# Optimization experiments

Hardware: AMD Instinct MI355X
Metric: run time of the kernel (lower is better)

Reference implementation:

```python
import jax, jax.numpy as jnp
import numpy as np

E = 2048      # embed_dim
H = 16        # num_heads
HD = E // H // 2   # differential head dim = 64
S = 2048      # seq len
B = 1         # batch
DEPTH = 12
LAMBDA_INIT = 0.8 - 0.6 * float(np.exp(-0.3 * DEPTH))
EPS = 1e-5


def setup_inputs() -> dict:
    key = jax.random.key(0)
    ks = jax.random.split(key, 12)
    n = lambda k, shape, s=1.0: (jax.random.normal(k, shape, dtype=jnp.float32) * s)
    return {
        "query": n(ks[0], (S, B, E)),
        "key": n(ks[1], (S, B, E)),
        "value": n(ks[2], (S, B, E)),
        "rel_pos": 0,
        "attn_mask": jnp.zeros((B, S), dtype=jnp.bool_),
        "Wq": n(ks[3], (E, E), 0.02),
        "Wk": n(ks[4], (E, E), 0.02),
        "Wv": n(ks[5], (E, E), 0.02),
        "Wo": n(ks[6], (E, E), 0.02),
        "lq1": n(ks[7], (HD,), 0.1),
        "lk1": n(ks[8], (HD,), 0.1),
        "lq2": n(ks[9], (HD,), 0.1),
        "lk2": n(ks[10], (HD,), 0.1),
        "subln_g": jnp.ones((2 * HD,), dtype=jnp.float32),
    }


def reference(query, key, value, rel_pos, attn_mask,
              Wq, Wk, Wv, Wo, lq1, lk1, lq2, lk2, subln_g):
    # (S,B,E) -> (B,S,E)
    q = jnp.einsum("sbe,fe->bsf", query, Wq)
    k = jnp.einsum("sbe,fe->bsf", key, Wk)
    v = jnp.einsum("sbe,fe->bsf", value, Wv)

    bsz, tgt_len, _ = q.shape
    scaling = HD ** -0.5

    q = q.reshape(bsz, tgt_len, 2 * H, HD).transpose(0, 2, 1, 3) * scaling  # (B,2H,S,hd)
    k = k.reshape(bsz, tgt_len, 2 * H, HD).transpose(0, 2, 1, 3)            # (B,2H,S,hd)
    v = v.reshape(bsz, tgt_len, H, 2 * HD).transpose(0, 2, 1, 3)            # (B,H,S,2hd)

    scores = jnp.einsum("bhqd,bhkd->bhqk", q, k)  # (B,2H,S,S)
    mask = jnp.where(attn_mask[:, None, None, :], -jnp.inf, 0.0).astype(scores.dtype)
    scores = jnp.nan_to_num(scores + mask)  # torch.nan_to_num: nan->0, -inf->finite min

    probs = jax.nn.softmax(scores.astype(jnp.float32), axis=-1).astype(scores.dtype)
    probs = jnp.clip(probs, -1e6, 1e6)  # clamp as in original (dropout is identity in eval)

    lam1 = jnp.exp(jnp.sum(lq1 * lk1))
    lam2 = jnp.exp(jnp.sum(lq2 * lk2))
    lam_full = lam1 - lam2 + LAMBDA_INIT

    probs = probs.reshape(bsz, H, 2, tgt_len, tgt_len)
    diff = probs[:, :, 0] - lam_full * probs[:, :, 1]   # (B,H,S,S)

    attn = jnp.einsum("bhqk,bhkd->bhqd", diff, v)       # (B,H,S,2hd)

    # RMSNorm over last dim with affine weight
    rms = jax.lax.rsqrt(jnp.mean(jnp.square(attn), axis=-1, keepdims=True) + EPS)
    attn = attn * rms * subln_g
    attn = attn * (1.0 - LAMBDA_INIT)

    attn = attn.transpose(0, 2, 1, 3).reshape(bsz, tgt_len, H * 2 * HD)  # (B,S,E)
    attn = attn.transpose(1, 0, 2)                                       # (S,B,E)
    return jnp.einsum("sbe,fe->sbf", attn, Wo)
```

## Files before the change

kernel.cpp:

```cpp
#include <hip/hip_runtime.h>
#include <stdint.h>

#define LAMBDA_INIT_F 0.7836057665f

typedef __bf16 bf16x8 __attribute__((ext_vector_type(8)));
typedef float  f32x4  __attribute__((ext_vector_type(4)));
typedef unsigned short u16x8 __attribute__((ext_vector_type(8)));
typedef unsigned short u16x4 __attribute__((ext_vector_type(4)));
typedef unsigned int u32x4 __attribute__((ext_vector_type(4)));

__device__ __forceinline__ unsigned short f2b(float f) {
    union { float f; unsigned u; } v; v.f = f;
    unsigned u = v.u;
    return (unsigned short)((u + 0x7fffu + ((u >> 16) & 1u)) >> 16);
}

__device__ __forceinline__ unsigned pk2(float a, float b) {
    unsigned ua = __float_as_uint(a) + 0x8000u;
    unsigned ub = __float_as_uint(b) + 0x8000u;
    return __builtin_amdgcn_perm(ub, ua, 0x07060302u);
}

#if __has_builtin(__builtin_amdgcn_exp2f)
#define EXP2(x) __builtin_amdgcn_exp2f(x)
#else
__device__ __forceinline__ float EXP2(float x) {
    float r; asm volatile("v_exp_f32 %0, %1\n\ts_nop 1" : "=v"(r) : "v"(x)); return r;
}
#endif

#define GLD16(gp, sp) __builtin_amdgcn_global_load_lds( \
    (const __attribute__((address_space(1))) void*)(uintptr_t)(gp), \
    (__attribute__((address_space(3))) void*)(uint32_t)(uintptr_t)(sp), 16, 0, 0)

__global__ __launch_bounds__(256) void cvt7(const float* __restrict__ s0, const float* __restrict__ s1,
                                            const float* __restrict__ s2, const float* __restrict__ s3,
                                            const float* __restrict__ s4, const float* __restrict__ s5,
                                            const float* __restrict__ s6,
                                            unsigned short* __restrict__ dst) {
    int z = blockIdx.y;
    const float* s = z == 0 ? s0 : z == 1 ? s1 : z == 2 ? s2 : z == 3 ? s3 : z == 4 ? s4 : z == 5 ? s5 : s6;
    unsigned short* d = dst + (size_t)z * 4194304;
    size_t i = ((size_t)blockIdx.x * 256 + threadIdx.x) * 8;
    float4 a = *(const float4*)(s + i);
    float4 b = *(const float4*)(s + i + 4);
    u16x8 o;
    o[0] = f2b(a.x); o[1] = f2b(a.y); o[2] = f2b(a.z); o[3] = f2b(a.w);
    o[4] = f2b(b.x); o[5] = f2b(b.y); o[6] = f2b(b.z); o[7] = f2b(b.w);
    *(u16x8*)(d + i) = o;
}

__global__ __launch_bounds__(512, 2) void gemm_qkv(const unsigned short* __restrict__ Abase,
                                                   const unsigned short* __restrict__ Bbase,
                                                   unsigned short* __restrict__ Cb,
                                                   unsigned short* __restrict__ VT,
                                                   float alpha0) {
    __shared__ __align__(16) unsigned short As[16384];
    __shared__ __align__(16) unsigned short Bs[16384];
    const int tid = threadIdx.x;
    const int wid = tid >> 6, lane = tid & 63;
    const int quad = lane >> 4, l16 = lane & 15;
    const int wr = wid >> 2, wc = wid & 3;
    const int bid = blockIdx.x;
    const int wrk = (bid & 7) * 24 + (bid >> 3);
    const int z = wrk >> 6;
    const int t6 = wrk & 63;
    const int m0 = (t6 >> 3) * 256, n0 = (t6 & 7) * 256;
    const unsigned short* A = Abase + (size_t)z * 4194304;
    const unsigned short* B = Bbase + (size_t)z * 4194304;
    const float alpha = (z == 0) ? alpha0 : 1.0f;

    const int sr = lane >> 2;
    const int sc = (((lane & 3) ^ ((lane >> 3) & 3)) * 8);
    const int rsw = ((l16 >> 1) & 3);

    f32x4 acc[8][4];
#pragma unroll
    for (int mi = 0; mi < 8; ++mi)
#pragma unroll
        for (int ni = 0; ni < 4; ++ni) acc[mi][ni] = f32x4{0.f, 0.f, 0.f, 0.f};

    auto STAGE_AH = [&](int h, int k0) {
        const int rowbase = (wid >> 2) * 128 + (wid & 3) * 16 + h * 64;
#pragma unroll
        for (int kk = 0; kk < 2; ++kk)
            GLD16(A + (size_t)(m0 + rowbase + sr) * 2048 + k0 + kk * 32 + sc, &As[(kk * 256 + rowbase) * 32]);
    };
    auto STAGE_BH = [&](int h, int k0) {
        const int rowbase = (wid >> 1) * 64 + (wid & 1) * 16 + h * 32;
#pragma unroll
        for (int kk = 0; kk < 2; ++kk)
            GLD16(B + (size_t)(n0 + rowbase + sr) * 2048 + k0 + kk * 32 + sc, &Bs[(kk * 256 + rowbase) * 32]);
    };

#define LD_A(mh, i, kk) (*(const bf16x8*)&As[(kk * 256 + wr * 128 + (mh) * 64 + (i) * 16 + l16) * 32 + (quad ^ rsw) * 8])
#define LD_B(nh, jn, kk) (*(const bf16x8*)&Bs[(kk * 256 + wc * 64 + (nh) * 32 + (jn) * 16 + l16) * 32 + (quad ^ rsw) * 8])

    STAGE_AH(0, 0); STAGE_BH(0, 0);
    STAGE_BH(1, 0);
    STAGE_AH(1, 0);
    asm volatile("s_waitcnt vmcnt(4)" ::: "memory");
    __builtin_amdgcn_s_barrier();

    for (int kt = 0; kt < 32; ++kt) {
        const int k1 = (kt + 1) * 64;
        bf16x8 af[2][4], b0[2][2], b1[2][2];

#pragma unroll
        for (int kk = 0; kk < 2; ++kk) {
#pragma unroll
            for (int i = 0; i < 4; ++i) af[kk][i] = LD_A(0, i, kk);
#pragma unroll
            for (int jn = 0; jn < 2; ++jn) b0[kk][jn] = LD_B(0, jn, kk);
        }
        __builtin_amdgcn_s_barrier();
        __builtin_amdgcn_s_setprio(1);
#pragma unroll
        for (int i = 0; i < 4; ++i)
#pragma unroll
            for (int jn = 0; jn < 2; ++jn)
#pragma unroll
                for (int kk = 0; kk < 2; ++kk)
                    acc[i][jn] = __builtin_amdgcn_mfma_f32_16x16x32_bf16(af[kk][i], b0[kk][jn], acc[i][jn], 0, 0, 0);
        __builtin_amdgcn_s_setprio(0);
        asm volatile("s_waitcnt vmcnt(2)" ::: "memory");
        __builtin_amdgcn_s_barrier();

#pragma unroll
        for (int kk = 0; kk < 2; ++kk)
#pragma unroll
            for (int jn = 0; jn < 2; ++jn) b1[kk][jn] = LD_B(1, jn, kk);
        if (kt < 31) { STAGE_AH(0, k1); STAGE_BH(0, k1); }
        __builtin_amdgcn_s_barrier();
        __builtin_amdgcn_s_setprio(1);
#pragma unroll
        for (int i = 0; i < 4; ++i)
#pragma unroll
            for (int jn = 0; jn < 2; ++jn)
#pragma unroll
                for (int kk = 0; kk < 2; ++kk)
                    acc[i][2 + jn] = __builtin_amdgcn_mfma_f32_16x16x32_bf16(af[kk][i], b1[kk][jn], acc[i][2 + jn], 0, 0, 0);
        __builtin_amdgcn_s_setprio(0);
        if (kt < 31) asm volatile("s_waitcnt vmcnt(4)" ::: "memory");
        else         asm volatile("s_waitcnt vmcnt(0)" ::: "memory");
        __builtin_amdgcn_s_barrier();

#pragma unroll
        for (int kk = 0; kk < 2; ++kk)
#pragma unroll
            for (int i = 0; i < 4; ++i) af[kk][i] = LD_A(1, i, kk);
        if (kt < 31) STAGE_BH(1, k1);
        __builtin_amdgcn_s_barrier();
        __builtin_amdgcn_s_setprio(1);
#pragma unroll
        for (int i = 0; i < 4; ++i)
#pragma unroll
            for (int jn = 0; jn < 2; ++jn)
#pragma unroll
                for (int kk = 0; kk < 2; ++kk)
                    acc[4 + i][2 + jn] = __builtin_amdgcn_mfma_f32_16x16x32_bf16(af[kk][i], b1[kk][jn], acc[4 + i][2 + jn], 0, 0, 0);
        __builtin_amdgcn_s_setprio(0);
        __builtin_amdgcn_s_barrier();

        if (kt < 31) STAGE_AH(1, k1);
        __builtin_amdgcn_s_barrier();
        __builtin_amdgcn_s_setprio(1);
#pragma unroll
        for (int i = 0; i < 4; ++i)
#pragma unroll
            for (int jn = 0; jn < 2; ++jn)
#pragma unroll
                for (int kk = 0; kk < 2; ++kk)
                    acc[4 + i][jn] = __builtin_amdgcn_mfma_f32_16x16x32_bf16(af[kk][i], b0[kk][jn], acc[4 + i][jn], 0, 0, 0);
        __builtin_amdgcn_s_setprio(0);
        asm volatile("s_waitcnt vmcnt(4)" ::: "memory");
        __builtin_amdgcn_s_barrier();
    }
#undef LD_A
#undef LD_B

    if (z == 2) {
#pragma unroll
        for (int mi = 0; mi < 8; ++mi)
#pragma unroll
            for (int ni = 0; ni < 4; ++ni) {
                int n = n0 + wc * 64 + ni * 16 + l16;
                int m = m0 + wr * 128 + mi * 16 + quad * 4;
                int sm = (m & ~31) | ((m & 12) << 1) | ((m & 16) >> 2) | (m & 3);
                u16x4 o;
#pragma unroll
                for (int r = 0; r < 4; ++r) o[r] = f2b(acc[mi][ni][r]);
                *(u16x4*)&VT[(size_t)n * 2048 + sm] = o;
            }
    } else {
        unsigned short* Cz = Cb + (size_t)z * 4194304;
#pragma unroll
        for (int mi = 0; mi < 8; ++mi)
#pragma unroll
            for (int ni = 0; ni < 4; ++ni)
#pragma unroll
                for (int r = 0; r < 4; ++r) {
                    int row = m0 + wr * 128 + mi * 16 + quad * 4 + r;
                    int col = n0 + wc * 64 + ni * 16 + l16;
                    Cz[(size_t)row * 2048 + col] = f2b(acc[mi][ni][r] * alpha);
                }
    }
}

template <int OUT_BF16, int NT, int DO_VT, int WPB>
__global__ __launch_bounds__(256, WPB) void gemm_bt(const unsigned short* __restrict__ Abase,
                                                    const unsigned short* __restrict__ Bbase,
                                                    void* __restrict__ Cbase,
                                                    unsigned short* __restrict__ VT,
                                                    float alpha0) {
    constexpr int MI = (NT == 128) ? 4 : 2;
    __shared__ __align__(16) unsigned short As[3][128 * 32];
    __shared__ __align__(16) unsigned short Bs[3][NT * 32];
    const int tid = threadIdx.x;
    const int w = tid >> 6, lane = tid & 63;
    const int quad = lane >> 4, l16 = lane & 15;
    const int b = blockIdx.z;
    const unsigned short* A = Abase + (size_t)b * 4194304;
    const unsigned short* B = Bbase + (size_t)b * 4194304;
    const float alpha = (b == 0) ? alpha0 : 1.0f;
    const int m0 = blockIdx.y * 128, n0 = blockIdx.x * NT;
    const int wm = (NT == 128) ? (w >> 1) * 64 : w * 32;
    const int wn = (NT == 128) ? (w & 1) * 64 : 0;
    const int sr = lane >> 2;
    const int sc = (((lane & 3) ^ ((lane >> 3) & 3)) * 8);
    const int rsw = ((l16 >> 1) & 3);

    f32x4 zz = {0.f, 0.f, 0.f, 0.f};
    f32x4 acc[MI][4];
#pragma unroll
    for (int i = 0; i < MI; ++i)
#pragma unroll
        for (int jn = 0; jn < 4; ++jn) acc[i][jn] = zz;

    auto STAGE = [&](int bsel, int k0) {
        GLD16(A + (size_t)(m0 + w * 16 + sr) * 2048 + k0 + sc,      &As[bsel][(w * 16) * 32]);
        GLD16(A + (size_t)(m0 + 64 + w * 16 + sr) * 2048 + k0 + sc, &As[bsel][(64 + w * 16) * 32]);
        if (NT == 128) {
            GLD16(B + (size_t)(n0 + w * 16 + sr) * 2048 + k0 + sc,      &Bs[bsel][(w * 16) * 32]);
            GLD16(B + (size_t)(n0 + 64 + w * 16 + sr) * 2048 + k0 + sc, &Bs[bsel][(64 + w * 16) * 32]);
        } else {
            GLD16(B + (size_t)(n0 + w * 16 + sr) * 2048 + k0 + sc, &Bs[bsel][(w * 16) * 32]);
        }
    };

    STAGE(0, 0);
    STAGE(1, 32);
    for (int c = 0; c < 64; ++c) {
        const int cur = c % 3;
        if (c < 62) {
            STAGE((c + 2) % 3, (c + 2) * 32);
            if (NT == 128) asm volatile("s_waitcnt vmcnt(8)" ::: "memory");
            else           asm volatile("s_waitcnt vmcnt(6)" ::: "memory");
        } else if (c == 62) {
            if (NT == 128) asm volatile("s_waitcnt vmcnt(4)" ::: "memory");
            else           asm volatile("s_waitcnt vmcnt(3)" ::: "memory");
        } else {
            asm volatile("s_waitcnt vmcnt(0)" ::: "memory");
        }
        __builtin_amdgcn_s_barrier();

        bf16x8 af[MI], bfr[4];
#pragma unroll
        for (int i = 0; i < MI; ++i) af[i]  = *(const bf16x8*)&As[cur][(wm + i * 16 + l16) * 32 + (quad ^ rsw) * 8];
#pragma unroll
        for (int i = 0; i < 4; ++i)  bfr[i] = *(const bf16x8*)&Bs[cur][(wn + i * 16 + l16) * 32 + (quad ^ rsw) * 8];
#pragma unroll
        for (int i = 0; i < MI; ++i)
#pragma unroll
            for (int jn = 0; jn < 4; ++jn)
                acc[i][jn] = __builtin_amdgcn_mfma_f32_16x16x32_bf16(af[i], bfr[jn], acc[i][jn], 0, 0, 0);
        __builtin_amdgcn_s_barrier();
    }

    if (DO_VT && b == 2) {
#pragma unroll
        for (int i = 0; i < MI; ++i)
#pragma unroll
            for (int jn = 0; jn < 4; ++jn) {
                int n = n0 + wn + jn * 16 + l16;
                int m = m0 + wm + i * 16 + quad * 4;
                int sm = (m & ~31) | ((m & 12) << 1) | ((m & 16) >> 2) | (m & 3);
                u16x4 o;
#pragma unroll
                for (int r = 0; r < 4; ++r) o[r] = f2b(acc[i][jn][r]);
                *(u16x4*)&VT[(size_t)n * 2048 + sm] = o;
            }
    } else {
#pragma unroll
        for (int i = 0; i < MI; ++i)
#pragma unroll
            for (int jn = 0; jn < 4; ++jn)
#pragma unroll
                for (int r = 0; r < 4; ++r) {
                    int row = m0 + wm + i * 16 + quad * 4 + r;
                    int col = n0 + wn + jn * 16 + l16;
                    float v = acc[i][jn][r] * alpha;
                    if (OUT_BF16)
                        ((unsigned short*)Cbase + (size_t)b * 4194304)[(size_t)row * 2048 + col] = f2b(v);
                    else
                        ((float*)Cbase)[(size_t)row * 2048 + col] = v;
                }
    }
}

__global__ __launch_bounds__(256, 2) void diff_attn(const unsigned short* __restrict__ qb,
                                                    const unsigned short* __restrict__ kb,
                                                    const unsigned short* __restrict__ vt,
                                                    const float* __restrict__ lq1,
                                                    const float* __restrict__ lk1,
                                                    const float* __restrict__ lq2,
                                                    const float* __restrict__ lk2,
                                                    const float* __restrict__ g,
                                                    unsigned short* __restrict__ Aout) {
    __shared__ __align__(16) unsigned short Ks[2][64 * 128];
    __shared__ __align__(16) unsigned short Vs[2][128 * 64];
    __shared__ float lam_s;
    const int tid = threadIdx.x, w = tid >> 6, lane = tid & 63;
    const int quad = lane >> 4, l16 = lane & 15;
    const int bid = blockIdx.x;
    const int wrk = (bid & 7) * 64 + (bid >> 3);
    const int j = wrk >> 5;
    const int q0 = (wrk & 31) * 64;

    if (tid < 64) {
        float p1 = lq1[tid] * lk1[tid];
        float p2 = lq2[tid] * lk2[tid];
        for (int off = 32; off; off >>= 1) { p1 += __shfl_xor(p1, off, 64); p2 += __shfl_xor(p2, off, 64); }
        if (tid == 0) lam_s = __expf(p1) - __expf(p2) + LAMBDA_INIT_F;
    }

    bf16x8 qf[2][2];
#pragma unroll
    for (int p = 0; p < 2; ++p)
#pragma unroll
        for (int dh = 0; dh < 2; ++dh)
            qf[p][dh] = *(const bf16x8*)&qb[(size_t)(q0 + w * 16 + l16) * 2048 + j * 128 + p * 64 + dh * 32 + quad * 8];

    f32x4 O[2][8];
#pragma unroll
    for (int p = 0; p < 2; ++p)
#pragma unroll
        for (int i = 0; i < 8; ++i)
#pragma unroll
            for (int r = 0; r < 4; ++r) O[p][i][r] = 0.f;
    float lsum[2] = {0.f, 0.f};

    const int srK = lane >> 4;
    const int srV = lane >> 3;
    const int scV = ((lane & 7) ^ (lane >> 3)) * 8;

    auto STAGE = [&](int bsel, int kv0) {
#pragma unroll
        for (int t = 0; t < 4; ++t) {
            int rowK = w * 16 + t * 4 + srK;
            int cbsK = ((lane & 15) ^ (rowK & 15)) * 8;
            GLD16(kb + (size_t)(kv0 + rowK) * 2048 + j * 128 + cbsK, &Ks[bsel][(w * 16 + t * 4) * 128]);
        }
#pragma unroll
        for (int t = 0; t < 4; ++t) {
            int rowV = w * 32 + t * 8 + srV;
            GLD16(vt + (size_t)(j * 128 + rowV) * 2048 + kv0 + scV, &Vs[bsel][(w * 32 + t * 8) * 64]);
        }
    };

    STAGE(0, 0);
    for (int c = 0; c < 32; ++c) {
        const int cur = c & 1;
        if (c < 31) {
            STAGE(cur ^ 1, (c + 1) * 64);
            asm volatile("s_waitcnt vmcnt(8)" ::: "memory");
        } else {
            asm volatile("s_waitcnt vmcnt(0)" ::: "memory");
        }
        __builtin_amdgcn_s_barrier();

        u32x4 pd[2][2];
#pragma unroll
        for (int p = 0; p < 2; ++p) {
#pragma unroll
            for (int i = 0; i < 4; ++i) {
                bf16x8 a0 = *(const bf16x8*)&Ks[cur][(i * 16 + l16) * 128 + ((p * 8 + quad) ^ l16) * 8];
                bf16x8 a1 = *(const bf16x8*)&Ks[cur][(i * 16 + l16) * 128 + ((p * 8 + 4 + quad) ^ l16) * 8];
                f32x4 s = {0.f, 0.f, 0.f, 0.f};
                s = __builtin_amdgcn_mfma_f32_16x16x32_bf16(a0, qf[p][0], s, 0, 0, 0);
                s = __builtin_amdgcn_mfma_f32_16x16x32_bf16(a1, qf[p][1], s, 0, 0, 0);
                float e0 = EXP2(s[0]), e1 = EXP2(s[1]), e2 = EXP2(s[2]), e3 = EXP2(s[3]);
                lsum[p] += (e0 + e1) + (e2 + e3);
                pd[p][i >> 1][(i & 1) * 2]     = pk2(e0, e1);
                pd[p][i >> 1][(i & 1) * 2 + 1] = pk2(e2, e3);
            }
        }
#pragma unroll
        for (int u = 0; u < 2; ++u) {
            const int blk = (((4 * u + quad) ^ (l16 & 7))) * 8;
#pragma unroll
            for (int dt = 0; dt < 8; ++dt) {
                bf16x8 vf8 = *(const bf16x8*)&Vs[cur][(dt * 16 + l16) * 64 + blk];
                O[0][dt] = __builtin_amdgcn_mfma_f32_16x16x32_bf16(vf8, __builtin_bit_cast(bf16x8, pd[0][u]), O[0][dt], 0, 0, 0);
                O[1][dt] = __builtin_amdgcn_mfma_f32_16x16x32_bf16(vf8, __builtin_bit_cast(bf16x8, pd[1][u]), O[1][dt], 0, 0, 0);
            }
        }
        __builtin_amdgcn_s_barrier();
    }

#pragma unroll
    for (int p = 0; p < 2; ++p) {
        lsum[p] += __shfl_xor(lsum[p], 16, 64);
        lsum[p] += __shfl_xor(lsum[p], 32, 64);
    }
    const float inv1 = 1.0f / lsum[0];
    const float inv2 = lam_s / lsum[1];

    float ssum = 0.f;
#pragma unroll
    for (int dt = 0; dt < 8; ++dt)
#pragma unroll
        for (int r = 0; r < 4; ++r) {
            float v = O[0][dt][r] * inv1 - O[1][dt][r] * inv2;
            O[0][dt][r] = v;
            ssum += v * v;
        }
    ssum += __shfl_xor(ssum, 16, 64);
    ssum += __shfl_xor(ssum, 32, 64);
    const float rms = rsqrtf(ssum * (1.0f / 128.0f) + 1e-5f) * (1.0f - LAMBDA_INIT_F);

#pragma unroll
    for (int dt = 0; dt < 8; ++dt) {
        float4 g4 = *(const float4*)&g[dt * 16 + quad * 4];
        u16x4 o;
        o[0] = f2b(O[0][dt][0] * rms * g4.x);
        o[1] = f2b(O[0][dt][1] * rms * g4.y);
        o[2] = f2b(O[0][dt][2] * rms * g4.z);
        o[3] = f2b(O[0][dt][3] * rms * g4.w);
        *(u16x4*)&Aout[(size_t)(q0 + w * 16 + l16) * 2048 + j * 128 + dt * 16 + quad * 4] = o;
    }
}

extern "C" void kernel_launch(void* const* d_in, const int* in_sizes, int n_in,
                              void* d_out, int out_size, void* d_ws, size_t ws_size,
                              hipStream_t stream) {
    const float* query = (const float*)d_in[0];
    const float* key   = (const float*)d_in[1];
    const float* value = (const float*)d_in[2];
    const float* Wq  = (const float*)d_in[5];
    const float* Wk  = (const float*)d_in[6];
    const float* Wv  = (const float*)d_in[7];
    const float* Wo  = (const float*)d_in[8];
    const float* lq1 = (const float*)d_in[9];
    const float* lk1 = (const float*)d_in[10];
    const float* lq2 = (const float*)d_in[11];
    const float* lk2 = (const float*)d_in[12];
    const float* g   = (const float*)d_in[13];

    char* ws = (char*)d_ws;
    const size_t MB = 1ull << 20;
    const size_t N4 = 4194304;
    unsigned short* qb  = (unsigned short*)(ws + 0 * MB);
    unsigned short* vt  = (unsigned short*)(ws + 16 * MB);
    unsigned short* Aat = (unsigned short*)(ws + 24 * MB);
    unsigned short* Xq  = (unsigned short*)(ws + 32 * MB);

    const float alpha_q = 0.125f * 1.44269504f;

    cvt7<<<dim3(2048, 7), dim3(256), 0, stream>>>(query, key, value, Wq, Wk, Wv, Wo, Xq);
    gemm_qkv<<<dim3(192), dim3(512), 0, stream>>>(Xq, Xq + 3 * N4, qb, vt, alpha_q);
    diff_attn<<<dim3(512), dim3(256), 0, stream>>>(qb, qb + N4, vt, lq1, lk1, lq2, lk2, g, Aat);
    gemm_bt<0, 64, 0, 2><<<dim3(32, 16, 1), dim3(256), 0, stream>>>(Aat, Xq + 6 * N4, d_out, nullptr, 1.0f);
}
```

Before: 301.5 us.

## Fuse fp32-to-bf16 conversion of QKV inputs and weights into the QKV GEMM loader

The separate conversion kernel now converts only Wo. The QKV GEMM reads fp32 activations and weights directly, converts them to bf16 in registers and writes them to LDS itself, replacing the direct global-to-LDS copies. Loads for the next k-tile are issued at the top of each iteration and stored to LDS in stages, with lgkmcnt waits instead of vmcnt waits. This removes the conversion pass's global read/write traffic and one launch. In exchange the GEMM reads twice as many bytes per tile and needs many more VGPRs for prefetch registers, which risks spills or lower occupancy under launch_bounds(512,2). It also rounds differently (round-half-up via pk2 rather than round-to-nearest-even).

```diff
diff --git a/kernel.cpp b/kernel.cpp
--- a/kernel.cpp
+++ b/kernel.cpp
@@ -50,8 +50,9 @@
     *(u16x8*)(d + i) = o;
 }
 
-__global__ __launch_bounds__(512, 2) void gemm_qkv(const unsigned short* __restrict__ Abase,
-                                                   const unsigned short* __restrict__ Bbase,
+__global__ __launch_bounds__(512, 2) void gemm_qkv(const float* __restrict__ Qf, const float* __restrict__ Kf,
+                                                   const float* __restrict__ Vf, const float* __restrict__ Wqf,
+                                                   const float* __restrict__ Wkf, const float* __restrict__ Wvf,
                                                    unsigned short* __restrict__ Cb,
                                                    unsigned short* __restrict__ VT,
                                                    float alpha0) {
@@ -66,8 +67,8 @@
     const int z = wrk >> 6;
     const int t6 = wrk & 63;
     const int m0 = (t6 >> 3) * 256, n0 = (t6 & 7) * 256;
-    const unsigned short* A = Abase + (size_t)z * 4194304;
-    const unsigned short* B = Bbase + (size_t)z * 4194304;
+    const float* Af = z == 0 ? Qf : z == 1 ? Kf : Vf;
+    const float* Bf = z == 0 ? Wqf : z == 1 ? Wkf : Wvf;
     const float alpha = (z == 0) ? alpha0 : 1.0f;
 
     const int sr = lane >> 2;
@@ -80,32 +81,63 @@
 #pragma unroll
         for (int ni = 0; ni < 4; ++ni) acc[mi][ni] = f32x4{0.f, 0.f, 0.f, 0.f};
 
-    auto STAGE_AH = [&](int h, int k0) {
-        const int rowbase = (wid >> 2) * 128 + (wid & 3) * 16 + h * 64;
-#pragma unroll
-        for (int kk = 0; kk < 2; ++kk)
-            GLD16(A + (size_t)(m0 + rowbase + sr) * 2048 + k0 + kk * 32 + sc, &As[(kk * 256 + rowbase) * 32]);
+    auto LOAD_A = [&](int h, int k0, f32x4 (&R)[2][2]) {
+        const int rb = (wid >> 2) * 128 + (wid & 3) * 16 + h * 64;
+#pragma unroll
+        for (int kk = 0; kk < 2; ++kk) {
+            const float* p = Af + (size_t)(m0 + rb + sr) * 2048 + k0 + kk * 32 + sc;
+            R[kk][0] = *(const f32x4*)p;
+            R[kk][1] = *(const f32x4*)(p + 4);
+        }
     };
-    auto STAGE_BH = [&](int h, int k0) {
-        const int rowbase = (wid >> 1) * 64 + (wid & 1) * 16 + h * 32;
-#pragma unroll
-        for (int kk = 0; kk < 2; ++kk)
-            GLD16(B + (size_t)(n0 + rowbase + sr) * 2048 + k0 + kk * 32 + sc, &Bs[(kk * 256 + rowbase) * 32]);
+    auto LOAD_B = [&](int h, int k0, f32x4 (&R)[2][2]) {
+        const int rb = (wid >> 1) * 64 + (wid & 1) * 16 + h * 32;
+#pragma unroll
+        for (int kk = 0; kk < 2; ++kk) {
+            const float* p = Bf + (size_t)(n0 + rb + sr) * 2048 + k0 + kk * 32 + sc;
+            R[kk][0] = *(const f32x4*)p;
+            R[kk][1] = *(const f32x4*)(p + 4);
+        }
+    };
+    auto WR_A = [&](int h, f32x4 (&R)[2][2]) {
+        const int rb = (wid >> 2) * 128 + (wid & 3) * 16 + h * 64;
+#pragma unroll
+        for (int kk = 0; kk < 2; ++kk) {
+            u32x4 o;
+            o[0] = pk2(R[kk][0][0], R[kk][0][1]); o[1] = pk2(R[kk][0][2], R[kk][0][3]);
+            o[2] = pk2(R[kk][1][0], R[kk][1][1]); o[3] = pk2(R[kk][1][2], R[kk][1][3]);
+            *(u32x4*)&As[(kk * 256 + rb) * 32 + lane * 8] = o;
+        }
+    };
+    auto WR_B = [&](int h, f32x4 (&R)[2][2]) {
+        const int rb = (wid >> 1) * 64 + (wid & 1) * 16 + h * 32;
+#pragma unroll
+        for (int kk = 0; kk < 2; ++kk) {
+            u32x4 o;
+            o[0] = pk2(R[kk][0][0], R[kk][0][1]); o[1] = pk2(R[kk][0][2], R[kk][0][3]);
+            o[2] = pk2(R[kk][1][0], R[kk][1][1]); o[3] = pk2(R[kk][1][2], R[kk][1][3]);
+            *(u32x4*)&Bs[(kk * 256 + rb) * 32 + lane * 8] = o;
+        }
     };
 
 #define LD_A(mh, i, kk) (*(const bf16x8*)&As[(kk * 256 + wr * 128 + (mh) * 64 + (i) * 16 + l16) * 32 + (quad ^ rsw) * 8])
 #define LD_B(nh, jn, kk) (*(const bf16x8*)&Bs[(kk * 256 + wc * 64 + (nh) * 32 + (jn) * 16 + l16) * 32 + (quad ^ rsw) * 8])
-
-    STAGE_AH(0, 0); STAGE_BH(0, 0);
-    STAGE_BH(1, 0);
-    STAGE_AH(1, 0);
-    asm volatile("s_waitcnt vmcnt(4)" ::: "memory");
-    __builtin_amdgcn_s_barrier();
+#define LGKM0 asm volatile("s_waitcnt lgkmcnt(0)" ::: "memory")
+
+    {
+        f32x4 pA0[2][2], pA1[2][2], pB0[2][2], pB1[2][2];
+        LOAD_A(0, 0, pA0); LOAD_B(0, 0, pB0); LOAD_B(1, 0, pB1); LOAD_A(1, 0, pA1);
+        WR_A(0, pA0); WR_B(0, pB0); WR_B(1, pB1); WR_A(1, pA1);
+        LGKM0;
+        __builtin_amdgcn_s_barrier();
+    }
 
     for (int kt = 0; kt < 32; ++kt) {
         const int k1 = (kt + 1) * 64;
         bf16x8 af[2][4], b0[2][2], b1[2][2];
-
+        f32x4 nA0[2][2], nA1[2][2], nB0[2][2], nB1[2][2];
+
+        if (kt < 31) { LOAD_A(0, k1, nA0); LOAD_B(0, k1, nB0); LOAD_B(1, k1, nB1); LOAD_A(1, k1, nA1); }
 #pragma unroll
         for (int kk = 0; kk < 2; ++kk) {
 #pragma unroll
@@ -123,14 +155,14 @@
                 for (int kk = 0; kk < 2; ++kk)
                     acc[i][jn] = __builtin_amdgcn_mfma_f32_16x16x32_bf16(af[kk][i], b0[kk][jn], acc[i][jn], 0, 0, 0);
         __builtin_amdgcn_s_setprio(0);
-        asm volatile("s_waitcnt vmcnt(2)" ::: "memory");
         __builtin_amdgcn_s_barrier();
 
 #pragma unroll
         for (int kk = 0; kk < 2; ++kk)
 #pragma unroll
             for (int jn = 0; jn < 2; ++jn) b1[kk][jn] = LD_B(1, jn, kk);
-        if (kt < 31) { STAGE_AH(0, k1); STAGE_BH(0, k1); }
+        if (kt < 31) { WR_A(0, nA0); WR_B(0, nB0); }
+        LGKM0;
         __builtin_amdgcn_s_barrier();
         __builtin_amdgcn_s_setprio(1);
 #pragma unroll
@@ -141,15 +173,14 @@
                 for (int kk = 0; kk < 2; ++kk)
                     acc[i][2 + jn] = __builtin_amdgcn_mfma_f32_16x16x32_bf16(af[kk][i], b1[kk][jn], acc[i][2 + jn], 0, 0, 0);
         __builtin_amdgcn_s_setprio(0);
-        if (kt < 31) asm volatile("s_waitcnt vmcnt(4)" ::: "memory");
-        else         asm volatile("s_waitcnt vmcnt(0)" ::: "memory");
         __builtin_amdgcn_s_barrier();
 
 #pragma unroll
         for (int kk = 0; kk < 2; ++kk)
 #pragma unroll
             for (int i = 0; i < 4; ++i) af[kk][i] = LD_A(1, i, kk);
-        if (kt < 31) STAGE_BH(1, k1);
+        if (kt < 31) WR_B(1, nB1);
+        LGKM0;
         __builtin_amdgcn_s_barrier();
         __builtin_amdgcn_s_setprio(1);
 #pragma unroll
@@ -162,7 +193,8 @@
         __builtin_amdgcn_s_setprio(0);
         __builtin_amdgcn_s_barrier();
 
-        if (kt < 31) STAGE_AH(1, k1);
+        if (kt < 31) WR_A(1, nA1);
+        LGKM0;
         __builtin_amdgcn_s_barrier();
         __builtin_amdgcn_s_setprio(1);
 #pragma unroll
@@ -173,11 +205,11 @@
                 for (int kk = 0; kk < 2; ++kk)
                     acc[4 + i][jn] = __builtin_amdgcn_mfma_f32_16x16x32_bf16(af[kk][i], b0[kk][jn], acc[4 + i][jn], 0, 0, 0);
         __builtin_amdgcn_s_setprio(0);
-        asm volatile("s_waitcnt vmcnt(4)" ::: "memory");
         __builtin_amdgcn_s_barrier();
     }
 #undef LD_A
 #undef LD_B
+#undef LGKM0
 
     if (z == 2) {
 #pragma unroll
@@ -463,12 +495,12 @@
     unsigned short* qb  = (unsigned short*)(ws + 0 * MB);
     unsigned short* vt  = (unsigned short*)(ws + 16 * MB);
     unsigned short* Aat = (unsigned short*)(ws + 24 * MB);
-    unsigned short* Xq  = (unsigned short*)(ws + 32 * MB);
+    unsigned short* WoB = (unsigned short*)(ws + 32 * MB);
 
     const float alpha_q = 0.125f * 1.44269504f;
 
-    cvt7<<<dim3(2048, 7), dim3(256), 0, stream>>>(query, key, value, Wq, Wk, Wv, Wo, Xq);
-    gemm_qkv<<<dim3(192), dim3(512), 0, stream>>>(Xq, Xq + 3 * N4, qb, vt, alpha_q);
+    cvt7<<<dim3(2048, 1), dim3(256), 0, stream>>>(Wo, Wo, Wo, Wo, Wo, Wo, Wo, WoB);
+    gemm_qkv<<<dim3(192), dim3(512), 0, stream>>>(query, key, value, Wq, Wk, Wv, qb, vt, alpha_q);
     diff_attn<<<dim3(512), dim3(256), 0, stream>>>(qb, qb + N4, vt, lq1, lk1, lq2, lk2, g, Aat);
-    gemm_bt<0, 64, 0, 2><<<dim3(32, 16, 1), dim3(256), 0, stream>>>(Aat, Xq + 6 * N4, d_out, nullptr, 1.0f);
-}
+    gemm_bt<0, 64, 0, 2><<<dim3(32, 16, 1), dim3(256), 0, stream>>>(Aat, WoB, d_out, nullptr, 1.0f);
+}
```

Result: slower. 392.2 us (+30.1%).

## Load V fragments directly from global memory and drop V shared staging

Applied to the files above, without the earlier changes.

The attention kernel no longer stages V tiles through LDS. Each lane loads its V fragments for the PV MFMAs straight from global memory into registers, which halves the shared memory footprint, and the launch bound is raised to allow three blocks per CU. The wait counts are adjusted to the new number of outstanding loads. The output projection GEMM also switches to a larger tile configuration with fewer blocks. The trade is higher register pressure and uncoalesced, latency-exposed global V reads that every wave repeats, in exchange for fewer LDS stores and barriers and more resident blocks.

```diff
diff --git a/kernel.cpp b/kernel.cpp
--- a/kernel.cpp
+++ b/kernel.cpp
@@ -308,7 +308,7 @@
     }
 }
 
-__global__ __launch_bounds__(256, 2) void diff_attn(const unsigned short* __restrict__ qb,
+__global__ __launch_bounds__(256, 3) void diff_attn(const unsigned short* __restrict__ qb,
                                                     const unsigned short* __restrict__ kb,
                                                     const unsigned short* __restrict__ vt,
                                                     const float* __restrict__ lq1,
@@ -318,7 +318,6 @@
                                                     const float* __restrict__ g,
                                                     unsigned short* __restrict__ Aout) {
     __shared__ __align__(16) unsigned short Ks[2][64 * 128];
-    __shared__ __align__(16) unsigned short Vs[2][128 * 64];
     __shared__ float lam_s;
     const int tid = threadIdx.x, w = tid >> 6, lane = tid & 63;
     const int quad = lane >> 4, l16 = lane & 15;
@@ -351,31 +350,30 @@
     float lsum[2] = {0.f, 0.f};
 
     const int srK = lane >> 4;
-    const int srV = lane >> 3;
-    const int scV = ((lane & 7) ^ (lane >> 3)) * 8;
-
-    auto STAGE = [&](int bsel, int kv0) {
+    const unsigned short* vrow = vt + (size_t)(j * 128 + l16) * 2048 + quad * 8;
+
+    auto STAGE_K = [&](int bsel, int kv0) {
 #pragma unroll
         for (int t = 0; t < 4; ++t) {
             int rowK = w * 16 + t * 4 + srK;
             int cbsK = ((lane & 15) ^ (rowK & 15)) * 8;
             GLD16(kb + (size_t)(kv0 + rowK) * 2048 + j * 128 + cbsK, &Ks[bsel][(w * 16 + t * 4) * 128]);
         }
-#pragma unroll
-        for (int t = 0; t < 4; ++t) {
-            int rowV = w * 32 + t * 8 + srV;
-            GLD16(vt + (size_t)(j * 128 + rowV) * 2048 + kv0 + scV, &Vs[bsel][(w * 32 + t * 8) * 64]);
-        }
     };
 
-    STAGE(0, 0);
+    STAGE_K(0, 0);
     for (int c = 0; c < 32; ++c) {
         const int cur = c & 1;
+        const int kv0 = c * 64;
+        bf16x8 vf0[8];
+#pragma unroll
+        for (int dt = 0; dt < 8; ++dt)
+            vf0[dt] = *(const bf16x8*)&vrow[(size_t)dt * 16 * 2048 + kv0];
         if (c < 31) {
-            STAGE(cur ^ 1, (c + 1) * 64);
+            STAGE_K(cur ^ 1, kv0 + 64);
+            asm volatile("s_waitcnt vmcnt(12)" ::: "memory");
+        } else {
             asm volatile("s_waitcnt vmcnt(8)" ::: "memory");
-        } else {
-            asm volatile("s_waitcnt vmcnt(0)" ::: "memory");
         }
         __builtin_amdgcn_s_barrier();
 
@@ -395,15 +393,17 @@
                 pd[p][i >> 1][(i & 1) * 2 + 1] = pk2(e2, e3);
             }
         }
-#pragma unroll
-        for (int u = 0; u < 2; ++u) {
-            const int blk = (((4 * u + quad) ^ (l16 & 7))) * 8;
-#pragma unroll
-            for (int dt = 0; dt < 8; ++dt) {
-                bf16x8 vf8 = *(const bf16x8*)&Vs[cur][(dt * 16 + l16) * 64 + blk];
-                O[0][dt] = __builtin_amdgcn_mfma_f32_16x16x32_bf16(vf8, __builtin_bit_cast(bf16x8, pd[0][u]), O[0][dt], 0, 0, 0);
-                O[1][dt] = __builtin_amdgcn_mfma_f32_16x16x32_bf16(vf8, __builtin_bit_cast(bf16x8, pd[1][u]), O[1][dt], 0, 0, 0);
-            }
+        bf16x8 vf1[8];
+#pragma unroll
+        for (int dt = 0; dt < 8; ++dt) {
+            vf1[dt] = *(const bf16x8*)&vrow[(size_t)dt * 16 * 2048 + kv0 + 32];
+            O[0][dt] = __builtin_amdgcn_mfma_f32_16x16x32_bf16(vf0[dt], __builtin_bit_cast(bf16x8, pd[0][0]), O[0][dt], 0, 0, 0);
+            O[1][dt] = __builtin_amdgcn_mfma_f32_16x16x32_bf16(vf0[dt], __builtin_bit_cast(bf16x8, pd[1][0]), O[1][dt], 0, 0, 0);
+        }
+#pragma unroll
+        for (int dt = 0; dt < 8; ++dt) {
+            O[0][dt] = __builtin_amdgcn_mfma_f32_16x16x32_bf16(vf1[dt], __builtin_bit_cast(bf16x8, pd[0][1]), O[0][dt], 0, 0, 0);
+            O[1][dt] = __builtin_amdgcn_mfma_f32_16x16x32_bf16(vf1[dt], __builtin_bit_cast(bf16x8, pd[1][1]), O[1][dt], 0, 0, 0);
         }
         __builtin_amdgcn_s_barrier();
     }
@@ -470,5 +470,5 @@
     cvt7<<<dim3(2048, 7), dim3(256), 0, stream>>>(query, key, value, Wq, Wk, Wv, Wo, Xq);
     gemm_qkv<<<dim3(192), dim3(512), 0, stream>>>(Xq, Xq + 3 * N4, qb, vt, alpha_q);
     diff_attn<<<dim3(512), dim3(256), 0, stream>>>(qb, qb + N4, vt, lq1, lk1, lq2, lk2, g, Aat);
-    gemm_bt<0, 64, 0, 2><<<dim3(32, 16, 1), dim3(256), 0, stream>>>(Aat, Xq + 6 * N4, d_out, nullptr, 1.0f);
-}
+    gemm_bt<0, 128, 0, 3><<<dim3(16, 16, 1), dim3(256), 0, stream>>>(Aat, Xq + 6 * N4, d_out, nullptr, 1.0f);
+}
```

Result: slower. 447.7 us (+48.5%).
